# Performance work log

Hardware: AMD Instinct MI355X
Metric: run time of the kernel (lower is better)

The kernel has to match this reference:

```python
import jax, jax.numpy as jnp
import numpy as np

NUM_HEADS = 12
LN_EPS = 1e-5


def _depthwise_conv(x, w):
    # x: [N, H, W, C], w: [kh, kw, 1, C] (HWIO, feature_group_count=C)
    return jax.lax.conv_general_dilated(
        x, w, window_strides=(1, 1), padding=((1, 1), (1, 1)),
        dimension_numbers=('NHWC', 'HWIO', 'NHWC'),
        feature_group_count=x.shape[-1])


def _pool_norm(t, w, g, b, T, H, W):
    # t: [B, nh, L, hd] -> depthwise 2D conv over (H, W) per frame, then LayerNorm(hd)
    B, nh, L, hd = t.shape
    x = t.reshape(B * nh * T, H, W, hd)
    x = _depthwise_conv(x, w)
    x = x.reshape(B, nh, L, hd)
    mu = x.mean(-1, keepdims=True)
    var = x.var(-1, keepdims=True)
    return (x - mu) / jnp.sqrt(var + LN_EPS) * g + b


def _forward(x, qkv_w, out_w, out_b, q_pool_w, k_pool_w, v_pool_w,
             q_ln_g, q_ln_b, k_ln_g, k_ln_b, v_ln_g, v_ln_b,
             rel_pos_h, rel_pos_w, T, H, W):
    B, L, C = x.shape
    nh = NUM_HEADS
    hd = C // nh
    scale = hd ** -0.5
    S = H * W

    # QKV projection (no bias), split into heads: [B, nh, L, hd]
    qkv = (x @ qkv_w.T).reshape(B, L, 3, nh, hd).transpose(2, 0, 3, 1, 4)
    q, k, v = qkv[0], qkv[1], qkv[2]

    # Conv pooling (stride 1, same padding) + LayerNorm per head channel dim
    q = _pool_norm(q, q_pool_w, q_ln_g, q_ln_b, T, H, W)
    k = _pool_norm(k, k_pool_w, k_ln_g, k_ln_b, T, H, W)
    v = _pool_norm(v, v_pool_w, v_ln_g, v_ln_b, T, H, W)

    # Scaled dot-product scores: [B, nh, L, L]
    attn = jnp.einsum('bhqd,bhkd->bhqk', q * scale, k)

    # Decomposed relative position bias, added per temporal block (diagonal in T)
    dist_h = jnp.arange(H)[:, None] - jnp.arange(H)[None, :] + (H - 1)
    dist_w = jnp.arange(W)[:, None] - jnp.arange(W)[None, :] + (W - 1)
    Rh = rel_pos_h[dist_h]  # [H, H, hd]
    Rw = rel_pos_w[dist_w]  # [W, W, hd]
    q5 = q.reshape(B, nh, T, H, W, hd)
    rel_h = jnp.einsum('bntxyc,xkc->bntxyk', q5, Rh)  # [B, nh, T, H, W, H]
    rel_w = jnp.einsum('bntxyc,ykc->bntxyk', q5, Rw)  # [B, nh, T, H, W, W]
    bias = rel_h[..., :, None] + rel_w[..., None, :]   # [B, nh, T, H, W, H, W]
    bias = bias.reshape(B, nh, T, S, S).transpose(2, 0, 1, 3, 4)  # [T, B, nh, S, S]

    attn6 = attn.reshape(B, nh, T, S, T, S)
    idx = jnp.arange(T)
    attn6 = attn6.at[:, :, idx, :, idx, :].add(bias)  # only diagonal temporal blocks
    attn = jax.nn.softmax(attn6.reshape(B, nh, L, L), axis=-1)

    out = jnp.einsum('bhqk,bhkd->bhqd', attn, v)
    out = out + q  # residual_pool
    out = out.transpose(0, 2, 1, 3).reshape(B, L, C)
    return out @ out_w.T + out_b


def setup_inputs() -> dict:
    key = jax.random.key(0)
    ks = jax.random.split(key, 12)
    B, T, H, W = 2, 2, 28, 28
    C, nh = 768, NUM_HEADS
    hd = C // nh
    L = T * H * W
    s = 0.02
    return {
        'x': jax.random.normal(ks[0], (B, L, C), jnp.float32),
        'qkv_w': jax.random.normal(ks[1], (3 * C, C), jnp.float32) * s,
        'out_w': jax.random.normal(ks[2], (C, C), jnp.float32) * s,
        'out_b': jnp.zeros((C,), jnp.float32),
        'q_pool_w': jax.random.normal(ks[3], (3, 3, 1, hd), jnp.float32) * s,
        'k_pool_w': jax.random.normal(ks[4], (3, 3, 1, hd), jnp.float32) * s,
        'v_pool_w': jax.random.normal(ks[5], (3, 3, 1, hd), jnp.float32) * s,
        'q_ln_g': jnp.ones((hd,), jnp.float32),
        'q_ln_b': jnp.zeros((hd,), jnp.float32),
        'k_ln_g': jnp.ones((hd,), jnp.float32),
        'k_ln_b': jnp.zeros((hd,), jnp.float32),
        'v_ln_g': jnp.ones((hd,), jnp.float32),
        'v_ln_b': jnp.zeros((hd,), jnp.float32),
        'rel_pos_h': jax.random.normal(ks[6], (2 * H - 1, hd), jnp.float32) * s,
        'rel_pos_w': jax.random.normal(ks[7], (2 * W - 1, hd), jnp.float32) * s,
        'T': T, 'H': H, 'W': W,
    }


def reference(x, qkv_w, out_w, out_b, q_pool_w, k_pool_w, v_pool_w,
              q_ln_g, q_ln_b, k_ln_g, k_ln_b, v_ln_g, v_ln_b,
              rel_pos_h, rel_pos_w, T, H, W):
    return _forward(x, qkv_w, out_w, out_b, q_pool_w, k_pool_w, v_pool_w,
                    q_ln_g, q_ln_b, k_ln_g, k_ln_b, v_ln_g, v_ln_b,
                    rel_pos_h, rel_pos_w, T, H, W)
```

## Files before the change

kernel.cpp:

```cpp
#include <hip/hip_runtime.h>
#include <math.h>

#define B_ 2
#define T_ 2
#define H_ 28
#define W_ 28
#define S_ (H_*W_)
#define L_ (T_*S_)
#define C_ 768
#define NH_ 12
#define HD_ 64
#define LN_EPS 1e-5f
#define LOG2E 1.4426950408889634f
#define SCALE_K (0.125f * LOG2E)

typedef unsigned int uint_;
typedef unsigned int u32x4 __attribute__((ext_vector_type(4)));
typedef __bf16 bf16x8 __attribute__((ext_vector_type(8)));
typedef float f32x4 __attribute__((ext_vector_type(4)));
typedef float f32x16 __attribute__((ext_vector_type(16)));

#define BC8(x) __builtin_bit_cast(bf16x8, (x))

__device__ __forceinline__ unsigned short f2bf(float f) {
  uint_ u = __builtin_bit_cast(uint_, f);
  u += 0x7FFFu + ((u >> 16) & 1u);
  return (unsigned short)(u >> 16);
}
__device__ __forceinline__ float bf2f(unsigned short h) {
  return __builtin_bit_cast(float, ((uint_)h) << 16);
}
__device__ __forceinline__ uint_ cvtpk(float a, float b) {
  uint_ r;
  asm("v_cvt_pk_bf16_f32 %0, %1, %2" : "=v"(r) : "v"(a), "v"(b));
  return r;
}
__device__ __forceinline__ void gload16(const void* g, void* l) {
  __builtin_amdgcn_global_load_lds(
      (const __attribute__((address_space(1))) unsigned int*)g,
      (__attribute__((address_space(3))) unsigned int*)l, 16, 0, 0);
}

__global__ __launch_bounds__(256) void cvt_all(
    const float* __restrict__ s0, int n0, unsigned short* __restrict__ d0,
    const float* __restrict__ s1, int n1, unsigned short* __restrict__ d1,
    const float* __restrict__ s2, int n2, unsigned short* __restrict__ d2) {
  int i = (blockIdx.x * 256 + threadIdx.x) * 8;
  const float* s; unsigned short* d;
  if (i < n0) { s = s0; d = d0; }
  else if (i < n0 + n1) { i -= n0; s = s1; d = d1; }
  else { i -= n0 + n1; if (i >= n2) return; s = s2; d = d2; }
  float4 a = *(const float4*)(s + i);
  float4 b = *(const float4*)(s + i + 4);
  u32x4 o;
  o.x = cvtpk(a.x, a.y); o.y = cvtpk(a.z, a.w);
  o.z = cvtpk(b.x, b.y); o.w = cvtpk(b.z, b.w);
  *(u32x4*)(d + i) = o;
}

__global__ __launch_bounds__(256) void cvt_rel(
    const float* __restrict__ rph, const float* __restrict__ rpw,
    unsigned short* __restrict__ Rhb, unsigned short* __restrict__ Rwb) {
  const int i = blockIdx.x * 256 + threadIdx.x;
  if (i >= 4096) return;
  const int j = i >> 6;
  const unsigned short vh = (j < 2*H_-1) ? f2bf(rph[i] * LOG2E) : 0;
  const unsigned short vw = (j < 2*W_-1) ? f2bf(rpw[i] * LOG2E) : 0;
  Rhb[i] = vh;
  Rwb[i] = vw;
}

__device__ __forceinline__ void gemm_core(
    const unsigned short* __restrict__ A, const unsigned short* __restrict__ Bm,
    int K, int m0, int n0, f32x4 (&acc)[4][4]) {
  __shared__ __align__(16) unsigned short As[128 * 32];
  __shared__ __align__(16) unsigned short Bs[128 * 32];
  const int tid = threadIdx.x;
  const int lane = tid & 63;
  const int wv = tid >> 6;
  const int wm = wv >> 1, wn = wv & 1;
  const int srow = tid >> 2, scol = (tid & 3) * 8;
  const int fr = lane & 15, fk = (lane >> 4) * 8;
  const unsigned short* ag = A + (size_t)(m0 + srow) * K + scol;
  const unsigned short* bg = Bm + (size_t)(n0 + srow) * K + scol;
  unsigned short* asd = As + tid * 8;
  unsigned short* bsd = Bs + tid * 8;
  const int arow = wm * 64 + fr;
  const int brow = wn * 64 + fr;
  for (int k0 = 0; k0 < K; k0 += 32) {
    __syncthreads();
    gload16(ag + k0, asd);
    gload16(ag + (size_t)64 * K + k0, asd + 2048);
    gload16(bg + k0, bsd);
    gload16(bg + (size_t)64 * K + k0, bsd + 2048);
    __syncthreads();
    bf16x8 af[4], bfr[4];
    #pragma unroll
    for (int m = 0; m < 4; ++m)
      af[m] = *(const bf16x8*)(As + (arow + m * 16) * 32 + fk);
    #pragma unroll
    for (int n = 0; n < 4; ++n)
      bfr[n] = *(const bf16x8*)(Bs + (brow + n * 16) * 32 + fk);
    #pragma unroll
    for (int m = 0; m < 4; ++m)
      #pragma unroll
      for (int n = 0; n < 4; ++n)
        acc[m][n] = __builtin_amdgcn_mfma_f32_16x16x32_bf16(af[m], bfr[n], acc[m][n], 0, 0, 0);
  }
}

__global__ __launch_bounds__(256) void qkv_gemm_mfma(
    const unsigned short* __restrict__ Xbf, const unsigned short* __restrict__ Wbf,
    float* __restrict__ q_raw, float* __restrict__ k_raw, float* __restrict__ v_raw) {
  f32x4 acc[4][4] = {};
  const int m0 = blockIdx.y * 128;
  const int n0 = blockIdx.x * 128;
  gemm_core(Xbf, Wbf, C_, m0, n0, acc);
  const int lane = threadIdx.x & 63;
  const int wv = threadIdx.x >> 6;
  const int wm = wv >> 1, wn = wv & 1;
  const int fr = lane & 15, fj = (lane >> 4) * 4;
  #pragma unroll
  for (int n = 0; n < 4; ++n) {
    const int gn = n0 + wn * 64 + n * 16 + fr;
    const int which = (gn >= 2 * C_) ? 2 : ((gn >= C_) ? 1 : 0);
    const int rem = gn - which * C_;
    const int h = rem >> 6, d = rem & 63;
    float* dst = (which == 0) ? q_raw : ((which == 1) ? k_raw : v_raw);
    #pragma unroll
    for (int m = 0; m < 4; ++m) {
      #pragma unroll
      for (int j = 0; j < 4; ++j) {
        const int gm = m0 + wm * 64 + m * 16 + fj + j;
        if (gm < B_ * L_) {
          const int b = (gm >= L_) ? 1 : 0;
          const int l = gm - b * L_;
          dst[(((size_t)b * NH_ + h) * L_ + l) * HD_ + d] = acc[m][n][j];
        }
      }
    }
  }
}

__global__ __launch_bounds__(256) void proj_gemm_mfma(
    const unsigned short* __restrict__ Abf, const unsigned short* __restrict__ Wobf,
    const float* __restrict__ bo, float* __restrict__ out) {
  f32x4 acc[4][4] = {};
  const int m0 = blockIdx.y * 128;
  const int n0 = blockIdx.x * 128;
  gemm_core(Abf, Wobf, C_, m0, n0, acc);
  const int lane = threadIdx.x & 63;
  const int wv = threadIdx.x >> 6;
  const int wm = wv >> 1, wn = wv & 1;
  const int fr = lane & 15, fj = (lane >> 4) * 4;
  #pragma unroll
  for (int n = 0; n < 4; ++n) {
    const int gn = n0 + wn * 64 + n * 16 + fr;
    const float bias = bo[gn];
    #pragma unroll
    for (int m = 0; m < 4; ++m) {
      #pragma unroll
      for (int j = 0; j < 4; ++j) {
        const int gm = m0 + wm * 64 + m * 16 + fj + j;
        if (gm < B_ * L_) out[(size_t)gm * C_ + gn] = acc[m][n][j] + bias;
      }
    }
  }
}

__global__ __launch_bounds__(256) void pool_ln_fused(
    const float* __restrict__ q_raw, const float* __restrict__ k_raw,
    const float* __restrict__ v_raw,
    const float* __restrict__ qw, const float* __restrict__ kw,
    const float* __restrict__ vw,
    const float* __restrict__ qg, const float* __restrict__ qb2,
    const float* __restrict__ kg, const float* __restrict__ kb2,
    const float* __restrict__ vg, const float* __restrict__ vb2,
    unsigned short* __restrict__ Qmain, unsigned short* __restrict__ Kpack,
    unsigned short* __restrict__ Vtmp) {
  const int which = blockIdx.y;
  const float* in = (which == 0) ? q_raw : (which == 1) ? k_raw : v_raw;
  const float* w  = (which == 0) ? qw : (which == 1) ? kw : vw;
  const float* g  = (which == 0) ? qg : (which == 1) ? kg : vg;
  const float* bb = (which == 0) ? qb2 : (which == 1) ? kb2 : vb2;
  const float scale = (which == 1) ? SCALE_K : 1.f;

  const int pair = blockIdx.x * 4 + (threadIdx.x >> 6);
  const int d = threadIdx.x & 63;
  const int row0 = pair * 2;
  const int bh = row0 / L_;
  const int l0  = row0 % L_;
  const int t  = l0 / S_;
  const int sq = l0 % S_;
  const int x = sq / W_, y = sq % W_;
  const float* base = in + ((size_t)bh * L_ + t * S_) * HD_ + d;

  float acc0 = 0.f, acc1 = 0.f;
  #pragma unroll
  for (int dx = 0; dx < 3; ++dx) {
    const int xx = x + dx - 1;
    if (xx < 0 || xx >= H_) continue;
    const float* rb = base + (size_t)xx * W_ * HD_;
    const float w0 = w[(dx*3 + 0) * HD_ + d];
    const float w1 = w[(dx*3 + 1) * HD_ + d];
    const float w2 = w[(dx*3 + 2) * HD_ + d];
    const float cm1 = (y > 0)      ? rb[(y-1) * HD_] : 0.f;
    const float c0  = rb[y * HD_];
    const float cp1 = rb[(y+1) * HD_];
    const float cp2 = (y+2 < W_)   ? rb[(y+2) * HD_] : 0.f;
    acc0 += cm1*w0 + c0*w1 + cp1*w2;
    acc1 += c0*w0 + cp1*w1 + cp2*w2;
  }
  float a1 = acc0, a2 = acc0*acc0, b1 = acc1, b2 = acc1*acc1;
  #pragma unroll
  for (int off = 32; off; off >>= 1) {
    a1 += __shfl_xor(a1, off);
    a2 += __shfl_xor(a2, off);
    b1 += __shfl_xor(b1, off);
    b2 += __shfl_xor(b2, off);
  }
  const float mu0 = a1 * (1.f / 64.f);
  const float var0 = a2 * (1.f / 64.f) - mu0 * mu0;
  const float mu1 = b1 * (1.f / 64.f);
  const float var1 = b2 * (1.f / 64.f) - mu1 * mu1;
  const float gd = g[d], bd = bb[d];
  const unsigned short v0 = f2bf(((acc0 - mu0) * rsqrtf(var0 + LN_EPS) * gd + bd) * scale);
  const unsigned short v1 = f2bf(((acc1 - mu1) * rsqrtf(var1 + LN_EPS) * gd + bd) * scale);

  if (which == 1) {
    const int kt = l0 >> 5;
    const int c = d >> 4;
    const int lane2 = (((d >> 3) & 1) << 5) | (l0 & 31);
    unsigned short* kp = Kpack + ((((size_t)bh * 49 + kt) * 4 + c) * 64 + lane2) * 8 + (d & 7);
    kp[0] = v0;
    kp[8] = v1;
  } else if (which == 0) {
    Qmain[(size_t)row0 * 64 + d]       = v0;
    Qmain[(size_t)(row0 + 1) * 64 + d] = v1;
  } else {
    Vtmp[(size_t)row0 * 64 + d]       = v0;
    Vtmp[(size_t)(row0 + 1) * 64 + d] = v1;
  }
}

__global__ __launch_bounds__(256) void vpack_kernel(
    const unsigned short* __restrict__ Vtmp, unsigned short* __restrict__ Vpack) {
  __shared__ unsigned short tile[32][72];
  const int bh = blockIdx.y;
  const int kt = blockIdx.x;
  const int l0 = kt * 32;
  const int t = threadIdx.x;
  {
    const int r = t >> 3, c8 = (t & 7) * 8;
    u32x4 v = *(const u32x4*)(Vtmp + ((size_t)bh * L_ + l0 + r) * 64 + c8);
    *(u32x4*)&tile[r][c8] = v;
  }
  __syncthreads();
  const int d = t >> 2, gq = t & 3;
  unsigned short o[8];
  #pragma unroll
  for (int i = 0; i < 8; ++i) o[i] = tile[gq*8 + i][d];
  u32x4 ov;
  ov.x = (uint_)o[0] | ((uint_)o[1] << 16);
  ov.y = (uint_)o[2] | ((uint_)o[3] << 16);
  ov.z = (uint_)o[4] | ((uint_)o[5] << 16);
  ov.w = (uint_)o[6] | ((uint_)o[7] << 16);
  const int c = ((d >> 5) << 1) | (gq >> 1);
  const int lane2 = ((gq & 1) << 5) | (d & 31);
  *(u32x4*)(Vpack + ((((size_t)bh * 49 + kt) * 4 + c) * 64 + lane2) * 8) = ov;
}

__global__ __launch_bounds__(64) void relpos_mfma(
    const unsigned short* __restrict__ Qmain,
    const unsigned short* __restrict__ Rhb,
    const unsigned short* __restrict__ Rwb,
    unsigned short* __restrict__ QbiasPack) {
  __shared__ float P[16][128];
  const int qt16 = blockIdx.x;
  const int bt = blockIdx.y;
  const int bh = bt >> 1, t = bt & 1;
  const int lane = threadIdx.x;
  const int fr = lane & 15, fk = (lane >> 4) * 8;

  const size_t rowbase = (size_t)bh * L_ + t * S_ + qt16 * 16;
  const unsigned short* arow = Qmain + (rowbase + fr) * 64 + fk;
  const bf16x8 a0 = *(const bf16x8*)(arow);
  const bf16x8 a1 = *(const bf16x8*)(arow + 32);

  f32x4 acch[4] = {}, accw[4] = {};
  #pragma unroll
  for (int n = 0; n < 4; ++n) {
    const unsigned short* bh_ = Rhb + (n * 16 + fr) * 64 + fk;
    const unsigned short* bw_ = Rwb + (n * 16 + fr) * 64 + fk;
    acch[n] = __builtin_amdgcn_mfma_f32_16x16x32_bf16(a0, *(const bf16x8*)bh_, acch[n], 0, 0, 0);
    acch[n] = __builtin_amdgcn_mfma_f32_16x16x32_bf16(a1, *(const bf16x8*)(bh_ + 32), acch[n], 0, 0, 0);
    accw[n] = __builtin_amdgcn_mfma_f32_16x16x32_bf16(a0, *(const bf16x8*)bw_, accw[n], 0, 0, 0);
    accw[n] = __builtin_amdgcn_mfma_f32_16x16x32_bf16(a1, *(const bf16x8*)(bw_ + 32), accw[n], 0, 0, 0);
  }
  #pragma unroll
  for (int n = 0; n < 4; ++n)
    #pragma unroll
    for (int j = 0; j < 4; ++j) {
      P[(lane >> 4) * 4 + j][n * 16 + fr]      = acch[n][j];
      P[(lane >> 4) * 4 + j][64 + n * 16 + fr] = accw[n][j];
    }
  __syncthreads();

  if (lane < 56) {
    const int e0 = lane * 2;
    const int tb = e0 / 56;
    const int tw0 = e0 % 56;
    const int cb = e0 >> 4;
    const int hi2 = (e0 >> 3) & 1;
    const int ee = e0 & 7;
    #pragma unroll
    for (int r = 0; r < 16; ++r) {
      const int gl = t * S_ + qt16 * 16 + r;
      const int sq = qt16 * 16 + r;
      const int x = sq / W_, y = sq % W_;
      float v0 = 0.f, v1 = 0.f;
      if (tb == t) {
        if (tw0 < 28) {
          v0 = P[r][x - tw0 + 27];
          v1 = P[r][x - tw0 + 26];
        } else {
          const int k0 = tw0 - 28;
          v0 = P[r][64 + y - k0 + 27];
          v1 = P[r][64 + y - k0 + 26];
        }
      }
      const int lane2 = (hi2 << 5) | (gl & 31);
      unsigned short* dst = QbiasPack +
          ((((size_t)bh * 49 + (gl >> 5)) * 7 + cb) * 64 + lane2) * 8 + ee;
      *(uint_*)dst = cvtpk(v0, v1);
    }
  }
}

__device__ __forceinline__ void load_k(
    const unsigned short* kbase, int kt,
    u32x4& k0, u32x4& k1, u32x4& k2, u32x4& k3) {
  const unsigned short* kp = kbase + (size_t)kt * 2048;
  k0 = *(const u32x4*)(kp);
  k1 = *(const u32x4*)(kp + 512);
  k2 = *(const u32x4*)(kp + 1024);
  k3 = *(const u32x4*)(kp + 1536);
}

__device__ __forceinline__ void load_v(
    const unsigned short* vbase, int kt,
    u32x4& va, u32x4& vb, u32x4& vc, u32x4& vd) {
  const unsigned short* vp = vbase + (size_t)kt * 2048;
  va = *(const u32x4*)(vp);
  vb = *(const u32x4*)(vp + 512);
  vc = *(const u32x4*)(vp + 1024);
  vd = *(const u32x4*)(vp + 1536);
}

template<bool BIAS>
__device__ __forceinline__ f32x16 qk_tile(
    int kt, int lo, int hi, const u32x4 (&qf)[4],
    const unsigned short* __restrict__ qbias,
    u32x4 k0, u32x4 k1, u32x4 k2, u32x4 k3) {
  f32x16 s = {};
  s = __builtin_amdgcn_mfma_f32_32x32x16_bf16(BC8(k0), BC8(qf[0]), s, 0, 0, 0);
  s = __builtin_amdgcn_mfma_f32_32x32x16_bf16(BC8(k1), BC8(qf[1]), s, 0, 0, 0);
  s = __builtin_amdgcn_mfma_f32_32x32x16_bf16(BC8(k2), BC8(qf[2]), s, 0, 0, 0);
  s = __builtin_amdgcn_mfma_f32_32x32x16_bf16(BC8(k3), BC8(qf[3]), s, 0, 0, 0);
  if (BIAS) {
    const int kr = kt * 32 + lo;
    const int t = (kr >= S_) ? 1 : 0;
    const int sk = kr - t * S_;
    const int x = sk / W_, y = sk - x * W_;
    const int p1 = t*56 + x;
    const int p2 = t*56 + 28 + y;
    const uint_ v1 = 0x3F80u << ((p1 & 1) << 4);
    const uint_ v2 = 0x3F80u << ((p2 & 1) << 4);
    const int g1 = p1 >> 3, g2 = p2 >> 3;
    const int w1 = (p1 >> 1) & 3, w2 = (p2 >> 1) & 3;
    #pragma unroll
    for (int c = 0; c < 7; ++c) {
      const int gg = 2*c + hi;
      u32x4 oh;
      oh.x = ((g1 == gg && w1 == 0) ? v1 : 0u) | ((g2 == gg && w2 == 0) ? v2 : 0u);
      oh.y = ((g1 == gg && w1 == 1) ? v1 : 0u) | ((g2 == gg && w2 == 1) ? v2 : 0u);
      oh.z = ((g1 == gg && w1 == 2) ? v1 : 0u) | ((g2 == gg && w2 == 2) ? v2 : 0u);
      oh.w = ((g1 == gg && w1 == 3) ? v1 : 0u) | ((g2 == gg && w2 == 3) ? v2 : 0u);
      const u32x4 qb = *(const u32x4*)(qbias + c * 512);
      s = __builtin_amdgcn_mfma_f32_32x32x16_bf16(BC8(oh), BC8(qb), s, 0, 0, 0);
    }
  }
  return s;
}

__device__ __forceinline__ void sm_pv(
    const f32x16& s,
    u32x4 va, u32x4 vb, u32x4 vc, u32x4 vd,
    f32x16& acc0, f32x16& acc1, float& l_run) {
  uint_ pw0, pw1, pw2, pw3, pw4, pw5, pw6, pw7;
  {
    float a, b;
    a = exp2f(s[0]);  b = exp2f(s[1]);  l_run += a+b; pw0 = cvtpk(a,b);
    a = exp2f(s[2]);  b = exp2f(s[3]);  l_run += a+b; pw1 = cvtpk(a,b);
    a = exp2f(s[4]);  b = exp2f(s[5]);  l_run += a+b; pw2 = cvtpk(a,b);
    a = exp2f(s[6]);  b = exp2f(s[7]);  l_run += a+b; pw3 = cvtpk(a,b);
    a = exp2f(s[8]);  b = exp2f(s[9]);  l_run += a+b; pw4 = cvtpk(a,b);
    a = exp2f(s[10]); b = exp2f(s[11]); l_run += a+b; pw5 = cvtpk(a,b);
    a = exp2f(s[12]); b = exp2f(s[13]); l_run += a+b; pw6 = cvtpk(a,b);
    a = exp2f(s[14]); b = exp2f(s[15]); l_run += a+b; pw7 = cvtpk(a,b);
  }
  auto sA = __builtin_amdgcn_permlane32_swap(pw0, pw2, false, false);
  auto sB = __builtin_amdgcn_permlane32_swap(pw1, pw3, false, false);
  auto sC = __builtin_amdgcn_permlane32_swap(pw4, pw6, false, false);
  auto sD = __builtin_amdgcn_permlane32_swap(pw5, pw7, false, false);
  u32x4 pa0, pa1;
  pa0.x = sA[0]; pa0.y = sB[0]; pa0.z = sA[1]; pa0.w = sB[1];
  pa1.x = sC[0]; pa1.y = sD[0]; pa1.z = sC[1]; pa1.w = sD[1];

  acc0 = __builtin_amdgcn_mfma_f32_32x32x16_bf16(BC8(pa0), BC8(va), acc0, 0, 0, 0);
  acc0 = __builtin_amdgcn_mfma_f32_32x32x16_bf16(BC8(pa1), BC8(vb), acc0, 0, 0, 0);
  acc1 = __builtin_amdgcn_mfma_f32_32x32x16_bf16(BC8(pa0), BC8(vc), acc1, 0, 0, 0);
  acc1 = __builtin_amdgcn_mfma_f32_32x32x16_bf16(BC8(pa1), BC8(vd), acc1, 0, 0, 0);
}

__device__ __forceinline__ bool bias_needed(int kt, int qt) {
  const int kmin = (kt * 32 >= S_) ? 1 : 0;
  const int kmax = (kt * 32 + 31 >= S_) ? 1 : 0;
  const int qmin = (qt * 32 >= S_) ? 1 : 0;
  const int qmax = (qt * 32 + 31 >= S_) ? 1 : 0;
  return (kmin <= qmax) && (qmin <= kmax);
}

__global__ __launch_bounds__(256) void attn_mfma(
    const unsigned short* __restrict__ Qmain, const unsigned short* __restrict__ QbiasPack,
    const unsigned short* __restrict__ Kpack, const unsigned short* __restrict__ Vpack,
    unsigned short* __restrict__ Abf) {
  __shared__ float red_acc[3][32][64];
  __shared__ float red_l[4][32];

  const int id0 = blockIdx.x;
  const int swz = (id0 & 7) * 147 + (id0 >> 3);
  const int qt = swz % 49;
  const int bh = swz / 49;

  const int lane = threadIdx.x & 63;
  const int wv = threadIdx.x >> 6;
  const int lo = lane & 31, hi = lane >> 5;
  const int q0 = qt * 32;

  const unsigned short* qrow = Qmain + ((size_t)bh * L_ + q0 + lo) * 64 + hi * 8;
  u32x4 qf[4];
  #pragma unroll
  for (int c = 0; c < 4; ++c) qf[c] = *(const u32x4*)(qrow + c * 16);
  const unsigned short* qbias = QbiasPack + ((size_t)bh * 49 + qt) * 3584 + lane * 8;

  const unsigned short* kbase = Kpack + (size_t)bh * 49 * 2048 + lane * 8;
  const unsigned short* vbase = Vpack + (size_t)bh * 49 * 2048 + lane * 8;

  f32x16 acc0 = {}, acc1 = {};
  float l_run = 0.f;
  const int nt = (49 - wv + 3) >> 2;

  #define KT(j) (wv + 4 * (j))
  #define QK(j, K0, K1, K2, K3) \
    (bias_needed(KT(j), qt) \
      ? qk_tile<true>(KT(j), lo, hi, qf, qbias, K0, K1, K2, K3) \
      : qk_tile<false>(KT(j), lo, hi, qf, qbias, K0, K1, K2, K3))

  u32x4 kA0, kA1, kA2, kA3, kB0, kB1, kB2, kB3;
  u32x4 va, vb, vc, vd;

  load_k(kbase, KT(0), kA0, kA1, kA2, kA3);
  load_k(kbase, KT(1), kB0, kB1, kB2, kB3);
  f32x16 s_prev = QK(0, kA0, kA1, kA2, kA3);

  int j = 1;
  for (; j + 1 < nt; j += 2) {
    load_v(vbase, KT(j - 1), va, vb, vc, vd);
    f32x16 s_cur = QK(j, kB0, kB1, kB2, kB3);
    load_k(kbase, KT(j + 1), kA0, kA1, kA2, kA3);
    sm_pv(s_prev, va, vb, vc, vd, acc0, acc1, l_run);
    s_prev = s_cur;
    load_v(vbase, KT(j), va, vb, vc, vd);
    f32x16 s_cur2 = QK(j + 1, kA0, kA1, kA2, kA3);
    const int pf = (j + 2 < nt) ? j + 2 : nt - 1;
    load_k(kbase, KT(pf), kB0, kB1, kB2, kB3);
    sm_pv(s_prev, va, vb, vc, vd, acc0, acc1, l_run);
    s_prev = s_cur2;
  }
  if (j < nt) {
    load_v(vbase, KT(j - 1), va, vb, vc, vd);
    f32x16 s_cur = QK(j, kB0, kB1, kB2, kB3);
    sm_pv(s_prev, va, vb, vc, vd, acc0, acc1, l_run);
    s_prev = s_cur;
  }
  load_v(vbase, KT(nt - 1), va, vb, vc, vd);
  sm_pv(s_prev, va, vb, vc, vd, acc0, acc1, l_run);
  #undef QK
  #undef KT

  l_run += __shfl_xor(l_run, 32);

  if (hi == 0) red_l[wv][lo] = l_run;
  if (wv >= 1) {
    #pragma unroll
    for (int r = 0; r < 16; ++r) {
      const int row = (r & 3) + 8*(r >> 2) + 4*hi;
      red_acc[wv-1][row][lo]      = acc0[r];
      red_acc[wv-1][row][32 + lo] = acc1[r];
    }
  }
  __syncthreads();
  if (wv == 0) {
    const int b = bh / NH_, h = bh % NH_;
    #pragma unroll
    for (int r = 0; r < 16; ++r) {
      const int row = (r & 3) + 8*(r >> 2) + 4*hi;
      const float inv = 1.0f / (red_l[0][row] + red_l[1][row] +
                                red_l[2][row] + red_l[3][row]);
      const float o0 = (acc0[r] + red_acc[0][row][lo] +
                        red_acc[1][row][lo] + red_acc[2][row][lo]) * inv;
      const float o1 = (acc1[r] + red_acc[0][row][32+lo] +
                        red_acc[1][row][32+lo] + red_acc[2][row][32+lo]) * inv;
      const size_t qoff = ((size_t)bh * L_ + q0 + row) * 64 + lo;
      const size_t ooff = ((size_t)(b * L_ + q0 + row)) * C_ + h * 64 + lo;
      Abf[ooff]      = f2bf(o0 + bf2f(Qmain[qoff]));
      Abf[ooff + 32] = f2bf(o1 + bf2f(Qmain[qoff + 32]));
    }
  }
}

extern "C" void kernel_launch(void* const* d_in, const int* in_sizes, int n_in,
                              void* d_out, int out_size, void* d_ws, size_t ws_size,
                              hipStream_t stream) {
  const float* x         = (const float*)d_in[0];
  const float* qkv_w     = (const float*)d_in[1];
  const float* out_w     = (const float*)d_in[2];
  const float* out_b     = (const float*)d_in[3];
  const float* q_pool_w  = (const float*)d_in[4];
  const float* k_pool_w  = (const float*)d_in[5];
  const float* v_pool_w  = (const float*)d_in[6];
  const float* q_ln_g    = (const float*)d_in[7];
  const float* q_ln_b    = (const float*)d_in[8];
  const float* k_ln_g    = (const float*)d_in[9];
  const float* k_ln_b    = (const float*)d_in[10];
  const float* v_ln_g    = (const float*)d_in[11];
  const float* v_ln_b    = (const float*)d_in[12];
  const float* rel_pos_h = (const float*)d_in[13];
  const float* rel_pos_w = (const float*)d_in[14];

  float* R = (float*)d_ws;
  const size_t NQ = (size_t)B_ * NH_ * L_ * HD_;
  float* q_raw = R;
  unsigned short* Abf = (unsigned short*)R;
  float* k_raw = R + NQ;
  unsigned short* Vpack = (unsigned short*)(R + NQ);
  float* v_raw = R + 2*NQ;
  const size_t D_off = 3*NQ;
  unsigned short* Xbf   = (unsigned short*)(R + D_off);
  unsigned short* Qmain = (unsigned short*)(R + D_off);
  const size_t E_off = D_off + 1228800;
  unsigned short* Kpack = (unsigned short*)(R + E_off);
  const size_t F_off = E_off + 1204224;
  unsigned short* Wbf  = (unsigned short*)(R + F_off);
  unsigned short* Vtmp = (unsigned short*)(R + F_off);
  const size_t G_off = F_off + 1204224;
  unsigned short* Wobf = (unsigned short*)(R + G_off);
  const size_t H_off = G_off + 294912;
  unsigned short* QbiasPack = (unsigned short*)(R + H_off);
  const size_t I_off = H_off + 2107392;
  unsigned short* Rhb = (unsigned short*)(R + I_off);
  unsigned short* Rwb = (unsigned short*)(R + I_off + 2048);

  cvt_all<<<2328, 256, 0, stream>>>(x, 3136*768, Xbf,
                                    qkv_w, 2304*768, Wbf,
                                    out_w, 768*768, Wobf);
  cvt_rel<<<16, 256, 0, stream>>>(rel_pos_h, rel_pos_w, Rhb, Rwb);
  qkv_gemm_mfma<<<dim3(18, 25), 256, 0, stream>>>(Xbf, Wbf, q_raw, k_raw, v_raw);
  pool_ln_fused<<<dim3(4704, 3), 256, 0, stream>>>(
      q_raw, k_raw, v_raw, q_pool_w, k_pool_w, v_pool_w,
      q_ln_g, q_ln_b, k_ln_g, k_ln_b, v_ln_g, v_ln_b, Qmain, Kpack, Vtmp);
  vpack_kernel<<<dim3(49, 24), 256, 0, stream>>>(Vtmp, Vpack);
  relpos_mfma<<<dim3(49, 48), 64, 0, stream>>>(Qmain, Rhb, Rwb, QbiasPack);
  attn_mfma<<<1176, 256, 0, stream>>>(Qmain, QbiasPack, Kpack, Vpack, Abf);
  proj_gemm_mfma<<<dim3(6, 25), 256, 0, stream>>>(Abf, Wobf, out_b, (float*)d_out);
}
```

Baseline: 139.7 us.

## Double-buffer GEMM LDS, fuse V packing into pool-LN, add MFMA setprio

The shared GEMM core gets two LDS buffers so the next K tile loads while the current one is consumed, which drops one barrier per iteration. The pool+LayerNorm kernel now writes V directly in the packed layout attention expects, removing the separate vpack kernel launch and the intermediate buffer round trip. s_setprio is raised around MFMA sequences in attention to favour matrix issue. The costs are doubled LDS use in the GEMM, which may lower occupancy, and scattered 4-byte stores for V.

```diff
diff --git a/kernel.cpp b/kernel.cpp
--- a/kernel.cpp
+++ b/kernel.cpp
@@ -73,8 +73,8 @@
 __device__ __forceinline__ void gemm_core(
     const unsigned short* __restrict__ A, const unsigned short* __restrict__ Bm,
     int K, int m0, int n0, f32x4 (&acc)[4][4]) {
-  __shared__ __align__(16) unsigned short As[128 * 32];
-  __shared__ __align__(16) unsigned short Bs[128 * 32];
+  __shared__ __align__(16) unsigned short As[2][128 * 32];
+  __shared__ __align__(16) unsigned short Bs[2][128 * 32];
   const int tid = threadIdx.x;
   const int lane = tid & 63;
   const int wv = tid >> 6;
@@ -83,29 +83,38 @@
   const int fr = lane & 15, fk = (lane >> 4) * 8;
   const unsigned short* ag = A + (size_t)(m0 + srow) * K + scol;
   const unsigned short* bg = Bm + (size_t)(n0 + srow) * K + scol;
-  unsigned short* asd = As + tid * 8;
-  unsigned short* bsd = Bs + tid * 8;
   const int arow = wm * 64 + fr;
   const int brow = wn * 64 + fr;
+  const int dst = tid * 8;
+
+  gload16(ag, As[0] + dst);
+  gload16(ag + (size_t)64 * K, As[0] + 2048 + dst);
+  gload16(bg, Bs[0] + dst);
+  gload16(bg + (size_t)64 * K, Bs[0] + 2048 + dst);
+
+  int cur = 0;
   for (int k0 = 0; k0 < K; k0 += 32) {
     __syncthreads();
-    gload16(ag + k0, asd);
-    gload16(ag + (size_t)64 * K + k0, asd + 2048);
-    gload16(bg + k0, bsd);
-    gload16(bg + (size_t)64 * K + k0, bsd + 2048);
-    __syncthreads();
+    if (k0 + 32 < K) {
+      const int nxt = cur ^ 1;
+      gload16(ag + k0 + 32, As[nxt] + dst);
+      gload16(ag + (size_t)64 * K + k0 + 32, As[nxt] + 2048 + dst);
+      gload16(bg + k0 + 32, Bs[nxt] + dst);
+      gload16(bg + (size_t)64 * K + k0 + 32, Bs[nxt] + 2048 + dst);
+    }
     bf16x8 af[4], bfr[4];
     #pragma unroll
     for (int m = 0; m < 4; ++m)
-      af[m] = *(const bf16x8*)(As + (arow + m * 16) * 32 + fk);
+      af[m] = *(const bf16x8*)(As[cur] + (arow + m * 16) * 32 + fk);
     #pragma unroll
     for (int n = 0; n < 4; ++n)
-      bfr[n] = *(const bf16x8*)(Bs + (brow + n * 16) * 32 + fk);
+      bfr[n] = *(const bf16x8*)(Bs[cur] + (brow + n * 16) * 32 + fk);
     #pragma unroll
     for (int m = 0; m < 4; ++m)
       #pragma unroll
       for (int n = 0; n < 4; ++n)
         acc[m][n] = __builtin_amdgcn_mfma_f32_16x16x32_bf16(af[m], bfr[n], acc[m][n], 0, 0, 0);
+    cur ^= 1;
   }
 }
 
@@ -177,7 +186,7 @@
     const float* __restrict__ kg, const float* __restrict__ kb2,
     const float* __restrict__ vg, const float* __restrict__ vb2,
     unsigned short* __restrict__ Qmain, unsigned short* __restrict__ Kpack,
-    unsigned short* __restrict__ Vtmp) {
+    unsigned short* __restrict__ Vpack) {
   const int which = blockIdx.y;
   const float* in = (which == 0) ? q_raw : (which == 1) ? k_raw : v_raw;
   const float* w  = (which == 0) ? qw : (which == 1) ? kw : vw;
@@ -238,36 +247,13 @@
     Qmain[(size_t)row0 * 64 + d]       = v0;
     Qmain[(size_t)(row0 + 1) * 64 + d] = v1;
   } else {
-    Vtmp[(size_t)row0 * 64 + d]       = v0;
-    Vtmp[(size_t)(row0 + 1) * 64 + d] = v1;
-  }
-}
-
-__global__ __launch_bounds__(256) void vpack_kernel(
-    const unsigned short* __restrict__ Vtmp, unsigned short* __restrict__ Vpack) {
-  __shared__ unsigned short tile[32][72];
-  const int bh = blockIdx.y;
-  const int kt = blockIdx.x;
-  const int l0 = kt * 32;
-  const int t = threadIdx.x;
-  {
-    const int r = t >> 3, c8 = (t & 7) * 8;
-    u32x4 v = *(const u32x4*)(Vtmp + ((size_t)bh * L_ + l0 + r) * 64 + c8);
-    *(u32x4*)&tile[r][c8] = v;
-  }
-  __syncthreads();
-  const int d = t >> 2, gq = t & 3;
-  unsigned short o[8];
-  #pragma unroll
-  for (int i = 0; i < 8; ++i) o[i] = tile[gq*8 + i][d];
-  u32x4 ov;
-  ov.x = (uint_)o[0] | ((uint_)o[1] << 16);
-  ov.y = (uint_)o[2] | ((uint_)o[3] << 16);
-  ov.z = (uint_)o[4] | ((uint_)o[5] << 16);
-  ov.w = (uint_)o[6] | ((uint_)o[7] << 16);
-  const int c = ((d >> 5) << 1) | (gq >> 1);
-  const int lane2 = ((gq & 1) << 5) | (d & 31);
-  *(u32x4*)(Vpack + ((((size_t)bh * 49 + kt) * 4 + c) * 64 + lane2) * 8) = ov;
+    const int kt = l0 >> 5;
+    const int c = ((d >> 5) << 1) | ((l0 >> 4) & 1);
+    const int lane2 = (((l0 >> 3) & 1) << 5) | (d & 31);
+    const int e = l0 & 7;
+    *(uint_*)(Vpack + ((((size_t)bh * 49 + kt) * 4 + c) * 64 + lane2) * 8 + e) =
+        (uint_)v0 | ((uint_)v1 << 16);
+  }
 }
 
 __global__ __launch_bounds__(64) void relpos_mfma(
@@ -363,6 +349,7 @@
     const unsigned short* __restrict__ qbias,
     u32x4 k0, u32x4 k1, u32x4 k2, u32x4 k3) {
   f32x16 s = {};
+  __builtin_amdgcn_s_setprio(1);
   s = __builtin_amdgcn_mfma_f32_32x32x16_bf16(BC8(k0), BC8(qf[0]), s, 0, 0, 0);
   s = __builtin_amdgcn_mfma_f32_32x32x16_bf16(BC8(k1), BC8(qf[1]), s, 0, 0, 0);
   s = __builtin_amdgcn_mfma_f32_32x32x16_bf16(BC8(k2), BC8(qf[2]), s, 0, 0, 0);
@@ -390,6 +377,7 @@
       s = __builtin_amdgcn_mfma_f32_32x32x16_bf16(BC8(oh), BC8(qb), s, 0, 0, 0);
     }
   }
+  __builtin_amdgcn_s_setprio(0);
   return s;
 }
 
@@ -417,10 +405,12 @@
   pa0.x = sA[0]; pa0.y = sB[0]; pa0.z = sA[1]; pa0.w = sB[1];
   pa1.x = sC[0]; pa1.y = sD[0]; pa1.z = sC[1]; pa1.w = sD[1];
 
+  __builtin_amdgcn_s_setprio(1);
   acc0 = __builtin_amdgcn_mfma_f32_32x32x16_bf16(BC8(pa0), BC8(va), acc0, 0, 0, 0);
   acc0 = __builtin_amdgcn_mfma_f32_32x32x16_bf16(BC8(pa1), BC8(vb), acc0, 0, 0, 0);
   acc1 = __builtin_amdgcn_mfma_f32_32x32x16_bf16(BC8(pa0), BC8(vc), acc1, 0, 0, 0);
   acc1 = __builtin_amdgcn_mfma_f32_32x32x16_bf16(BC8(pa1), BC8(vd), acc1, 0, 0, 0);
+  __builtin_amdgcn_s_setprio(0);
 }
 
 __device__ __forceinline__ bool bias_needed(int kt, int qt) {
@@ -554,7 +544,6 @@
   float* q_raw = R;
   unsigned short* Abf = (unsigned short*)R;
   float* k_raw = R + NQ;
-  unsigned short* Vpack = (unsigned short*)(R + NQ);
   float* v_raw = R + 2*NQ;
   const size_t D_off = 3*NQ;
   unsigned short* Xbf   = (unsigned short*)(R + D_off);
@@ -562,8 +551,8 @@
   const size_t E_off = D_off + 1228800;
   unsigned short* Kpack = (unsigned short*)(R + E_off);
   const size_t F_off = E_off + 1204224;
-  unsigned short* Wbf  = (unsigned short*)(R + F_off);
-  unsigned short* Vtmp = (unsigned short*)(R + F_off);
+  unsigned short* Wbf   = (unsigned short*)(R + F_off);
+  unsigned short* Vpack = (unsigned short*)(R + F_off);
   const size_t G_off = F_off + 1204224;
   unsigned short* Wobf = (unsigned short*)(R + G_off);
   const size_t H_off = G_off + 294912;
@@ -579,8 +568,7 @@
   qkv_gemm_mfma<<<dim3(18, 25), 256, 0, stream>>>(Xbf, Wbf, q_raw, k_raw, v_raw);
   pool_ln_fused<<<dim3(4704, 3), 256, 0, stream>>>(
       q_raw, k_raw, v_raw, q_pool_w, k_pool_w, v_pool_w,
-      q_ln_g, q_ln_b, k_ln_g, k_ln_b, v_ln_g, v_ln_b, Qmain, Kpack, Vtmp);
-  vpack_kernel<<<dim3(49, 24), 256, 0, stream>>>(Vtmp, Vpack);
+      q_ln_g, q_ln_b, k_ln_g, k_ln_b, v_ln_g, v_ln_b, Qmain, Kpack, Vpack);
   relpos_mfma<<<dim3(49, 48), 64, 0, stream>>>(Qmain, Rhb, Rwb, QbiasPack);
   attn_mfma<<<1176, 256, 0, stream>>>(Qmain, QbiasPack, Kpack, Vpack, Abf);
   proj_gemm_mfma<<<dim3(6, 25), 256, 0, stream>>>(Abf, Wobf, out_b, (float*)d_out);
```

New measurement: 141.6 us. About the same (+1.3%).
